# Kernel tuning notes

Hardware: AMD Instinct MI355X
Metric: run time of the kernel (lower is better)

The kernel has to match this reference:

```python
import jax, jax.numpy as jnp
import numpy as np

EMBED_DIM = 1024
NUM_HEADS = 16
D_K = EMBED_DIM // NUM_HEADS


def setup_inputs() -> dict:
    key = jax.random.key(0)
    kx, kq, kk, kv, ko = jax.random.split(key, 5)
    scale = 1.0 / np.sqrt(EMBED_DIM)
    x = jax.random.normal(kx, (4, 2048, EMBED_DIM), dtype=jnp.float32)
    # Linear(embed_dim, embed_dim, bias=False) weights, stored [out, in] like torch
    Wq = jax.random.uniform(kq, (EMBED_DIM, EMBED_DIM), jnp.float32, -scale, scale)
    Wk = jax.random.uniform(kk, (EMBED_DIM, EMBED_DIM), jnp.float32, -scale, scale)
    Wv = jax.random.uniform(kv, (EMBED_DIM, EMBED_DIM), jnp.float32, -scale, scale)
    Wo = jax.random.uniform(ko, (EMBED_DIM, EMBED_DIM), jnp.float32, -scale, scale)
    return {"x": x, "Wq": Wq, "Wk": Wk, "Wv": Wv, "Wo": Wo}


def reference(x, Wq, Wk, Wv, Wo):
    b, s, _ = x.shape
    # torch Linear: y = x @ W.T
    def proj(W):
        y = jnp.einsum('bse,fe->bsf', x, W)
        return y.reshape(b, s, NUM_HEADS, D_K).transpose(0, 2, 1, 3)  # [b,h,s,d]
    q, k, v = proj(Wq), proj(Wk), proj(Wv)
    scores = jnp.einsum('bhqd,bhkd->bhqk', q, k) / jnp.sqrt(jnp.float32(D_K))
    attn = jax.nn.softmax(scores, axis=-1)  # dropout is identity in eval
    out = jnp.einsum('bhqk,bhkd->bhqd', attn, v)
    out = out.transpose(0, 2, 1, 3).reshape(b, s, EMBED_DIM)
    return jnp.einsum('bsf,ef->bse', out, Wo)
```

## Files before the change

kernel.cpp:

```cpp
#include <hip/hip_runtime.h>
#include <hip/hip_bf16.h>

typedef unsigned short u16;
typedef unsigned int   u32;
typedef __attribute__((ext_vector_type(8))) __bf16 bf16x8;
typedef __attribute__((ext_vector_type(2))) __bf16 bf16x2;
typedef __attribute__((ext_vector_type(8))) u16    ushort8v;
typedef __attribute__((ext_vector_type(4))) short  short4v;
typedef __attribute__((ext_vector_type(2))) float  f32x2;
typedef __attribute__((ext_vector_type(4))) float  floatx4;

#define EMBED 1024
#define SEQ   2048
#define BATCH 4
#define NH    16
#define DKH   64
#define BHN   (BATCH*NH)
#define ZSTRIDE ((size_t)BHN*SEQ*DKH)

__device__ __forceinline__ u16 f2bf(float f){
  union { float f; unsigned u; } v; v.f = f;
  unsigned r = (v.u + 0x7FFFu + ((v.u >> 16) & 1u)) >> 16;
  return (u16)r;
}
__device__ __forceinline__ u32 pk2(float a, float b){
  f32x2 v = {a, b};
  return __builtin_bit_cast(u32, __builtin_convertvector(v, bf16x2));
}

__device__ __forceinline__ bf16x8 ld_frag(const u16* p){
  return __builtin_bit_cast(bf16x8, *(const ushort8v*)p);
}

__device__ __forceinline__ floatx4 mfma16(bf16x8 a, bf16x8 b, floatx4 c){
  return __builtin_amdgcn_mfma_f32_16x16x32_bf16(a, b, c, 0, 0, 0);
}
__device__ __forceinline__ floatx4 mfma_pv(short4v a, short4v b, floatx4 c){
  return __builtin_amdgcn_mfma_f32_16x16x16bf16_1k(a, b, c, 0, 0, 0);
}

__device__ __forceinline__ void gl_lds16(const u16* g, u16* l){
  __builtin_amdgcn_global_load_lds((const __attribute__((address_space(1))) void*)g,
                                   (__attribute__((address_space(3))) void*)l,
                                   16, 0, 0);
}

__global__ __launch_bounds__(256) void cvt_all(const float* __restrict__ x,
    const float* __restrict__ wq, const float* __restrict__ wk,
    const float* __restrict__ wv, const float* __restrict__ wo,
    u16* __restrict__ Xb, u16* __restrict__ Wqb, u16* __restrict__ Wkb,
    u16* __restrict__ Wvb, u16* __restrict__ Wob){
  int b = blockIdx.x;
  const float* src; u16* dst; int i;
  if (b < 8192){ src = x; dst = Xb; i = b*256 + threadIdx.x; }
  else {
    int k = (b - 8192) >> 10, r = (b - 8192) & 1023;
    src = (k==0) ? wq : (k==1) ? wk : (k==2) ? wv : wo;
    dst = (k==0) ? Wqb : (k==1) ? Wkb : (k==2) ? Wvb : Wob;
    i = r*256 + threadIdx.x;
  }
  float4 v = ((const float4*)src)[i];
  ushort4 o;
  o.x = f2bf(v.x); o.y = f2bf(v.y); o.z = f2bf(v.z); o.w = f2bf(v.w);
  ((ushort4*)dst)[i] = o;
}

__device__ __forceinline__ void gemm_core(const u16* Abase, const u16* Bbase,
                                          u16* As, u16* Bs, floatx4 acc[4][4]){
  const int tid  = threadIdx.x;
  const int lane = tid & 63, w = tid >> 6;
  const int lm   = lane & 15, quad = lane >> 4;
  const int wm   = (w & 1) * 64, wn = (w >> 1) * 64;

  #pragma unroll
  for (int mi = 0; mi < 4; ++mi)
    #pragma unroll
    for (int ni = 0; ni < 4; ++ni)
      acc[mi][ni] = (floatx4){0.f, 0.f, 0.f, 0.f};

  for (int kt = 0; kt < EMBED/32; ++kt){
    const int k0 = kt * 32;
    __syncthreads();
    #pragma unroll
    for (int r = 0; r < 2; ++r){
      int i = r*256 + tid;
      int row = i >> 2, kc = i & 3;
      gl_lds16(Abase + (size_t)row*EMBED + k0 + kc*8, As + i*8);
      gl_lds16(Bbase + (size_t)row*EMBED + k0 + kc*8, Bs + i*8);
    }
    __syncthreads();
    bf16x8 af[4], bf[4];
    #pragma unroll
    for (int mi = 0; mi < 4; ++mi)
      af[mi] = ld_frag(&As[(wm + mi*16 + lm)*32 + quad*8]);
    #pragma unroll
    for (int ni = 0; ni < 4; ++ni)
      bf[ni] = ld_frag(&Bs[(wn + ni*16 + lm)*32 + quad*8]);
    #pragma unroll
    for (int mi = 0; mi < 4; ++mi)
      #pragma unroll
      for (int ni = 0; ni < 4; ++ni)
        acc[mi][ni] = mfma16(af[mi], bf[ni], acc[mi][ni]);
  }
}

#define QSCALE 0.1803368801111204f
__global__ __launch_bounds__(256) void gemm_qkv(const u16* __restrict__ X,
    const u16* __restrict__ Wq, const u16* __restrict__ Wk, const u16* __restrict__ Wv,
    u16* __restrict__ QKV){
  __shared__ __attribute__((aligned(16))) u16 As[128*32];
  __shared__ __attribute__((aligned(16))) u16 Bs[128*32];
  const int z  = blockIdx.z;
  const u16* W = (z == 0) ? Wq : (z == 1) ? Wk : Wv;
  const int m0 = blockIdx.y * 128, n0 = blockIdx.x * 128;
  floatx4 acc[4][4];
  gemm_core(X + (size_t)m0*EMBED, W + (size_t)n0*EMBED, As, Bs, acc);

  const int tid = threadIdx.x, lane = tid & 63, w = tid >> 6;
  const int lm = lane & 15, quad = lane >> 4;
  const int wm = (w & 1) * 64, wn = (w >> 1) * 64;
  u16* outz = QKV + (size_t)z * ZSTRIDE;

  if (z == 2){
    #pragma unroll
    for (int mi = 0; mi < 4; ++mi)
      #pragma unroll
      for (int ni = 0; ni < 4; ++ni){
        int mbase = m0 + wm + mi*16 + quad*4;
        int n = n0 + wn + ni*16 + lm;
        int b = mbase >> 11, sb = mbase & 2047;
        int h = n >> 6, d = n & 63;
        u16* dst = outz + (((size_t)(b*NH + h))*DKH + d)*SEQ + sb;
        uint2 pv;
        pv.x = pk2(acc[mi][ni][0], acc[mi][ni][1]);
        pv.y = pk2(acc[mi][ni][2], acc[mi][ni][3]);
        *reinterpret_cast<uint2*>(dst) = pv;
      }
  } else {
    const float scale = (z == 0) ? QSCALE : 1.0f;
    #pragma unroll
    for (int mi = 0; mi < 4; ++mi)
      #pragma unroll
      for (int ni = 0; ni < 4; ++ni)
        #pragma unroll
        for (int r = 0; r < 4; ++r){
          int m = m0 + wm + mi*16 + quad*4 + r;
          int n = n0 + wn + ni*16 + lm;
          int b = m >> 11, s = m & 2047, h = n >> 6, d = n & 63;
          outz[(((size_t)(b*NH + h))*SEQ + s)*DKH + d] = f2bf(acc[mi][ni][r] * scale);
        }
  }
}

__global__ __launch_bounds__(256) void gemm_out(const u16* __restrict__ A,
    const u16* __restrict__ W, float* __restrict__ C){
  __shared__ __attribute__((aligned(16))) u16 As[128*32];
  __shared__ __attribute__((aligned(16))) u16 Bs[128*32];
  const int m0 = blockIdx.y * 128, n0 = blockIdx.x * 128;
  floatx4 acc[4][4];
  gemm_core(A + (size_t)m0*EMBED, W + (size_t)n0*EMBED, As, Bs, acc);

  const int tid = threadIdx.x, lane = tid & 63, w = tid >> 6;
  const int lm = lane & 15, quad = lane >> 4;
  const int wm = (w & 1) * 64, wn = (w >> 1) * 64;
  #pragma unroll
  for (int mi = 0; mi < 4; ++mi)
    #pragma unroll
    for (int ni = 0; ni < 4; ++ni)
      #pragma unroll
      for (int r = 0; r < 4; ++r){
        int m = m0 + wm + mi*16 + quad*4 + r;
        int n = n0 + wn + ni*16 + lm;
        C[(size_t)m*EMBED + n] = acc[mi][ni][r];
      }
}

#define KSS 520
__global__ __launch_bounds__(256, 4) void attn_kernel(const u16* __restrict__ QKV,
                                                      u16* __restrict__ Out){
  __shared__ __attribute__((aligned(16))) u16 Ks[2][8*KSS];
  __shared__ __attribute__((aligned(16))) u16 Vs[2][64*64];

  const int tid = threadIdx.x, lane = tid & 63, w = tid >> 6;
  const int lm = lane & 15, quad = lane >> 4;
  const int bh = blockIdx.x;
  const int q0 = blockIdx.y * 128;
  const u16* Qh = QKV + (size_t)bh * SEQ * DKH;
  const u16* Kh = QKV + ZSTRIDE + (size_t)bh * SEQ * DKH;
  const u16* Vh = QKV + 2*ZSTRIDE + (size_t)bh * DKH * SEQ;

  const int sK = tid & 63, cK = tid >> 6;
  const int dV = tid >> 3, gV = tid & 7;
  const size_t vsrc0 = (size_t)dV * SEQ + ((gV ^ (dV & 7)) * 8);
  const size_t vsrc1 = vsrc0 + (size_t)32 * SEQ;

  bf16x8 qf[2][2];
  #pragma unroll
  for (int qt = 0; qt < 2; ++qt)
    #pragma unroll
    for (int st = 0; st < 2; ++st)
      qf[qt][st] = ld_frag(Qh + (size_t)(q0 + w*32 + qt*16 + lm)*DKH + st*32 + quad*8);

  const short4v ones4 = {0x3F80, 0x3F80, 0x3F80, 0x3F80};

  floatx4 o[2][4], lac[2];
  #pragma unroll
  for (int qt = 0; qt < 2; ++qt){
    lac[qt] = (floatx4){0.f, 0.f, 0.f, 0.f};
    #pragma unroll
    for (int dt = 0; dt < 4; ++dt) o[qt][dt] = (floatx4){0.f, 0.f, 0.f, 0.f};
  }

  gl_lds16(Kh + (size_t)sK*DKH + cK*8,     Ks[0] + cK*KSS + sK*8);
  gl_lds16(Kh + (size_t)sK*DKH + (cK+4)*8, Ks[0] + (cK+4)*KSS + sK*8);
  gl_lds16(Vh + vsrc0,                     Vs[0] + tid*8);
  gl_lds16(Vh + vsrc1,                     Vs[0] + 2048 + tid*8);

  for (int kt = 0; kt < SEQ/64; ++kt){
    const int cur = kt & 1;
    __syncthreads();
    if (kt + 1 < SEQ/64){
      const int nk0 = (kt + 1) * 64;
      gl_lds16(Kh + (size_t)(nk0 + sK)*DKH + cK*8,     Ks[cur^1] + cK*KSS + sK*8);
      gl_lds16(Kh + (size_t)(nk0 + sK)*DKH + (cK+4)*8, Ks[cur^1] + (cK+4)*KSS + sK*8);
      gl_lds16(Vh + vsrc0 + nk0,                       Vs[cur^1] + tid*8);
      gl_lds16(Vh + vsrc1 + nk0,                       Vs[cur^1] + 2048 + tid*8);
    }
    const u16* Kc = Ks[cur];
    const u16* Vc = Vs[cur];

    #pragma unroll
    for (int t = 0; t < 4; ++t){
      bf16x8 kf0 = ld_frag(&Kc[quad*KSS     + (t*16 + lm)*8]);
      bf16x8 kf1 = ld_frag(&Kc[(quad+4)*KSS + (t*16 + lm)*8]);
      short4v pf[2];
      #pragma unroll
      for (int qt = 0; qt < 2; ++qt){
        floatx4 s = (floatx4){0.f,0.f,0.f,0.f};
        s = mfma16(kf0, qf[qt][0], s);
        s = mfma16(kf1, qf[qt][1], s);
        uint2 p;
        p.x = pk2(__builtin_amdgcn_exp2f(s[0]), __builtin_amdgcn_exp2f(s[1]));
        p.y = pk2(__builtin_amdgcn_exp2f(s[2]), __builtin_amdgcn_exp2f(s[3]));
        pf[qt] = __builtin_bit_cast(short4v, p);
      }
      lac[0] = mfma_pv(pf[0], ones4, lac[0]);
      lac[1] = mfma_pv(pf[1], ones4, lac[1]);
      const int cg = ((t*2 + (quad >> 1)) ^ (lm & 7)) * 8 + (quad & 1) * 4;
      #pragma unroll
      for (int dt = 0; dt < 4; ++dt){
        short4v vb = __builtin_bit_cast(short4v,
                        *(const uint2*)(Vc + (dt*16 + lm)*64 + cg));
        o[0][dt] = mfma_pv(pf[0], vb, o[0][dt]);
        o[1][dt] = mfma_pv(pf[1], vb, o[1][dt]);
      }
    }
  }

  const int bI = bh >> 4, h = bh & 15;
  #pragma unroll
  for (int qt = 0; qt < 2; ++qt){
    floatx4 inv;
    #pragma unroll
    for (int r = 0; r < 4; ++r) inv[r] = __builtin_amdgcn_rcpf(lac[qt][r]);
    #pragma unroll
    for (int dt = 0; dt < 4; ++dt)
      #pragma unroll
      for (int r = 0; r < 4; ++r){
        int s = q0 + w*32 + qt*16 + quad*4 + r;
        Out[((size_t)(bI*SEQ + s))*EMBED + h*DKH + dt*16 + lm] = f2bf(o[qt][dt][r] * inv[r]);
      }
  }
}

extern "C" void kernel_launch(void* const* d_in, const int* in_sizes, int n_in,
                              void* d_out, int out_size, void* d_ws, size_t ws_size,
                              hipStream_t stream){
  const float* x  = (const float*)d_in[0];
  const float* Wq = (const float*)d_in[1];
  const float* Wk = (const float*)d_in[2];
  const float* Wv = (const float*)d_in[3];
  const float* Wo = (const float*)d_in[4];
  float* out = (float*)d_out;

  char* ws = (char*)d_ws;
  u16* Xb  = (u16*)ws;
  u16* Wqb = (u16*)(ws + (size_t)16777216);
  u16* Wkb = Wqb + 1048576;
  u16* Wvb = Wkb + 1048576;
  u16* Wob = Wvb + 1048576;
  u16* QKV = (u16*)(ws + (size_t)25165824);
  u16* At  = (u16*)(ws + (size_t)75497472);

  cvt_all<<<12288, 256, 0, stream>>>(x, Wq, Wk, Wv, Wo, Xb, Wqb, Wkb, Wvb, Wob);
  gemm_qkv<<<dim3(8, 64, 3), 256, 0, stream>>>(Xb, Wqb, Wkb, Wvb, QKV);
  attn_kernel<<<dim3(64, 16), 256, 0, stream>>>(QKV, At);
  gemm_out<<<dim3(8, 64), 256, 0, stream>>>(At, Wob, out);
}
```

Baseline: 284.8 us.

## Double-buffer LDS tiles in GEMM kernels and remap grid to M-major order

```diff
diff --git a/kernel.cpp b/kernel.cpp
--- a/kernel.cpp
+++ b/kernel.cpp
@@ -65,12 +65,14 @@
   ((ushort4*)dst)[i] = o;
 }
 
-__device__ __forceinline__ void gemm_core(const u16* Abase, const u16* Bbase,
-                                          u16* As, u16* Bs, floatx4 acc[4][4]){
+__device__ __forceinline__ void gemm_core_db(const u16* Abase, const u16* Bbase,
+                                             u16* As, u16* Bs, floatx4 acc[4][4]){
   const int tid  = threadIdx.x;
   const int lane = tid & 63, w = tid >> 6;
   const int lm   = lane & 15, quad = lane >> 4;
   const int wm   = (w & 1) * 64, wn = (w >> 1) * 64;
+  const int row0 = tid >> 2, kc = tid & 3;
+  const int row1 = (256 + tid) >> 2;
 
   #pragma unroll
   for (int mi = 0; mi < 4; ++mi)
@@ -78,24 +80,32 @@
     for (int ni = 0; ni < 4; ++ni)
       acc[mi][ni] = (floatx4){0.f, 0.f, 0.f, 0.f};
 
+  gl_lds16(Abase + (size_t)row0*EMBED + kc*8, As + tid*8);
+  gl_lds16(Bbase + (size_t)row0*EMBED + kc*8, Bs + tid*8);
+  gl_lds16(Abase + (size_t)row1*EMBED + kc*8, As + (256 + tid)*8);
+  gl_lds16(Bbase + (size_t)row1*EMBED + kc*8, Bs + (256 + tid)*8);
+
   for (int kt = 0; kt < EMBED/32; ++kt){
-    const int k0 = kt * 32;
+    const int cur = kt & 1;
     __syncthreads();
-    #pragma unroll
-    for (int r = 0; r < 2; ++r){
-      int i = r*256 + tid;
-      int row = i >> 2, kc = i & 3;
-      gl_lds16(Abase + (size_t)row*EMBED + k0 + kc*8, As + i*8);
-      gl_lds16(Bbase + (size_t)row*EMBED + k0 + kc*8, Bs + i*8);
+    if (kt + 1 < EMBED/32){
+      const int k0 = (kt + 1) * 32;
+      u16* Ad = As + (cur^1)*128*32;
+      u16* Bd = Bs + (cur^1)*128*32;
+      gl_lds16(Abase + (size_t)row0*EMBED + k0 + kc*8, Ad + tid*8);
+      gl_lds16(Bbase + (size_t)row0*EMBED + k0 + kc*8, Bd + tid*8);
+      gl_lds16(Abase + (size_t)row1*EMBED + k0 + kc*8, Ad + (256 + tid)*8);
+      gl_lds16(Bbase + (size_t)row1*EMBED + k0 + kc*8, Bd + (256 + tid)*8);
     }
-    __syncthreads();
+    const u16* Ac = As + cur*128*32;
+    const u16* Bc = Bs + cur*128*32;
     bf16x8 af[4], bf[4];
     #pragma unroll
     for (int mi = 0; mi < 4; ++mi)
-      af[mi] = ld_frag(&As[(wm + mi*16 + lm)*32 + quad*8]);
+      af[mi] = ld_frag(&Ac[(wm + mi*16 + lm)*32 + quad*8]);
     #pragma unroll
     for (int ni = 0; ni < 4; ++ni)
-      bf[ni] = ld_frag(&Bs[(wn + ni*16 + lm)*32 + quad*8]);
+      bf[ni] = ld_frag(&Bc[(wn + ni*16 + lm)*32 + quad*8]);
     #pragma unroll
     for (int mi = 0; mi < 4; ++mi)
       #pragma unroll
@@ -108,13 +118,13 @@
 __global__ __launch_bounds__(256) void gemm_qkv(const u16* __restrict__ X,
     const u16* __restrict__ Wq, const u16* __restrict__ Wk, const u16* __restrict__ Wv,
     u16* __restrict__ QKV){
-  __shared__ __attribute__((aligned(16))) u16 As[128*32];
-  __shared__ __attribute__((aligned(16))) u16 Bs[128*32];
-  const int z  = blockIdx.z;
+  __shared__ __attribute__((aligned(16))) u16 As[2*128*32];
+  __shared__ __attribute__((aligned(16))) u16 Bs[2*128*32];
+  const int z  = blockIdx.y >> 3;
   const u16* W = (z == 0) ? Wq : (z == 1) ? Wk : Wv;
-  const int m0 = blockIdx.y * 128, n0 = blockIdx.x * 128;
+  const int m0 = blockIdx.x * 128, n0 = (blockIdx.y & 7) * 128;
   floatx4 acc[4][4];
-  gemm_core(X + (size_t)m0*EMBED, W + (size_t)n0*EMBED, As, Bs, acc);
+  gemm_core_db(X + (size_t)m0*EMBED, W + (size_t)n0*EMBED, As, Bs, acc);
 
   const int tid = threadIdx.x, lane = tid & 63, w = tid >> 6;
   const int lm = lane & 15, quad = lane >> 4;
@@ -154,11 +164,11 @@
 
 __global__ __launch_bounds__(256) void gemm_out(const u16* __restrict__ A,
     const u16* __restrict__ W, float* __restrict__ C){
-  __shared__ __attribute__((aligned(16))) u16 As[128*32];
-  __shared__ __attribute__((aligned(16))) u16 Bs[128*32];
-  const int m0 = blockIdx.y * 128, n0 = blockIdx.x * 128;
+  __shared__ __attribute__((aligned(16))) u16 As[2*128*32];
+  __shared__ __attribute__((aligned(16))) u16 Bs[2*128*32];
+  const int m0 = blockIdx.x * 128, n0 = blockIdx.y * 128;
   floatx4 acc[4][4];
-  gemm_core(A + (size_t)m0*EMBED, W + (size_t)n0*EMBED, As, Bs, acc);
+  gemm_core_db(A + (size_t)m0*EMBED, W + (size_t)n0*EMBED, As, Bs, acc);
 
   const int tid = threadIdx.x, lane = tid & 63, w = tid >> 6;
   const int lm = lane & 15, quad = lane >> 4;
@@ -293,7 +303,7 @@
   u16* At  = (u16*)(ws + (size_t)75497472);
 
   cvt_all<<<12288, 256, 0, stream>>>(x, Wq, Wk, Wv, Wo, Xb, Wqb, Wkb, Wvb, Wob);
-  gemm_qkv<<<dim3(8, 64, 3), 256, 0, stream>>>(Xb, Wqb, Wkb, Wvb, QKV);
+  gemm_qkv<<<dim3(64, 24), 256, 0, stream>>>(Xb, Wqb, Wkb, Wvb, QKV);
   attn_kernel<<<dim3(64, 16), 256, 0, stream>>>(QKV, At);
-  gemm_out<<<dim3(8, 64), 256, 0, stream>>>(At, Wob, out);
-}
+  gemm_out<<<dim3(64, 8), 256, 0, stream>>>(At, Wob, out);
+}
```

Measured after the change: 277.0 us. 1.03x faster.
